# Performance work log

Hardware: AMD Instinct MI355X
Metric: run time of the kernel (lower is better)

Reference implementation:

```python
import jax, jax.numpy as jnp
import numpy as np

N_NODES = 100000  # same count for users and items
N_EDGES = 4000000
D = 64
EPS = 1e-12


def setup_inputs() -> dict:
    key = jax.random.key(0)
    ks = jax.random.split(key, 8)
    return {
        "user_feat": jax.random.normal(ks[0], (N_NODES, D), dtype=jnp.float32),
        "item_feat": jax.random.normal(ks[1], (N_NODES, D), dtype=jnp.float32),
        "norm_ui": jax.random.uniform(ks[2], (N_EDGES, 1), dtype=jnp.float32),
        "norm_iu": jax.random.uniform(ks[3], (N_EDGES, 1), dtype=jnp.float32),
        "src_ui": jax.random.randint(ks[4], (N_EDGES,), 0, N_NODES, dtype=jnp.int32),
        "dst_ui": jax.random.randint(ks[5], (N_EDGES,), 0, N_NODES, dtype=jnp.int32),
        "src_iu": jax.random.randint(ks[6], (N_EDGES,), 0, N_NODES, dtype=jnp.int32),
        "dst_iu": jax.random.randint(ks[7], (N_EDGES,), 0, N_NODES, dtype=jnp.int32),
    }


def _l2_normalize(x):
    # F.normalize(x, dim=1, p=2): x / max(||x||_2, eps)
    n = jnp.sqrt(jnp.sum(x * x, axis=1, keepdims=True))
    return x / jnp.maximum(n, EPS)


def reference(user_feat, item_feat, norm_ui, norm_iu, src_ui, dst_ui, src_iu, dst_iu):
    # per-edge gather + scale (messages), then scatter-sum to destination nodes
    item_h = jax.ops.segment_sum(norm_ui * user_feat[src_ui], dst_ui, num_segments=N_NODES)
    user_h = jax.ops.segment_sum(norm_iu * item_feat[src_iu], dst_iu, num_segments=N_NODES)
    # per-node-type L2 normalize; stack [user_h, item_h] -> [2, N, D]
    return jnp.stack([_l2_normalize(user_h), _l2_normalize(item_h)])
```

## Files before the change

kernel.cpp:

```cpp
#include <hip/hip_runtime.h>

#define DFEAT 64
#define EPS 1e-12f
#define BPB 64
#define MAXB 3200
#define QPT 4
#define LSORT_CAP 3264


__device__ __forceinline__ unsigned pack_src_w(int s, float w) {
    unsigned u = __float_as_uint(w) + 0x8000u;
    return (((u >> 16) & 0x7FFFu) << 17) | (unsigned)s;
}
__device__ __forceinline__ int unpack_src(unsigned p) { return (int)(p & 0x1FFFFu); }
__device__ __forceinline__ float unpack_w(unsigned p) {
    return __uint_as_float(((p >> 17) & 0x7FFFu) << 16);
}

__global__ void zero_int_kernel(int* __restrict__ p, int n) {
    int i = blockIdx.x * blockDim.x + threadIdx.x;
    if (i < n) p[i] = 0;
}

__global__ __launch_bounds__(256, 6) void partition_kernel(
        const int* __restrict__ src_ui,
        const int* __restrict__ dst_ui,
        const float* __restrict__ norm_ui,
        const int* __restrict__ src_iu,
        const int* __restrict__ dst_iu,
        const float* __restrict__ norm_iu,
        int* __restrict__ cursor,
        unsigned* __restrict__ srcw,
        unsigned char* __restrict__ binlo,
        int n_edges, int n_nodes,
        int nbuckets, int cap) {
    __shared__ int cnt[MAXB];
    __shared__ int basearr[MAXB];
    const int tid = threadIdx.x;
    const long long total = 2LL * n_edges;
    const long long qbase = (long long)blockIdx.x * (256 * QPT);

    for (int c = tid; c < nbuckets; c += 256) cnt[c] = 0;
    __syncthreads();

    for (int k = 0; k < QPT; ++k) {
        long long q = qbase + (long long)k * 256 + tid;
        long long g0 = q << 2;
        if (g0 >= total) continue;
        if (g0 + 3 < total && (g0 + 3 < n_edges || g0 >= n_edges)) {
            const bool iu = (g0 >= n_edges);
            long long e0 = iu ? (g0 - n_edges) : g0;
            int4 d = *reinterpret_cast<const int4*>((iu ? dst_iu : dst_ui) + e0);
            int boff = iu ? n_nodes : 0;
            atomicAdd(&cnt[(d.x + boff) >> 6], 1);
            atomicAdd(&cnt[(d.y + boff) >> 6], 1);
            atomicAdd(&cnt[(d.z + boff) >> 6], 1);
            atomicAdd(&cnt[(d.w + boff) >> 6], 1);
        } else {
            for (long long g = g0; g < g0 + 4 && g < total; ++g) {
                int bin = (g < n_edges) ? dst_ui[g]
                                        : n_nodes + dst_iu[g - n_edges];
                atomicAdd(&cnt[bin >> 6], 1);
            }
        }
    }
    __syncthreads();

    for (int c = tid; c < nbuckets; c += 256) {
        int n = cnt[c];
        basearr[c] = (n > 0) ? atomicAdd(&cursor[c], n) : 0;
    }
    __syncthreads();
    for (int c = tid; c < nbuckets; c += 256) cnt[c] = 0;
    __syncthreads();

    auto place = [&](int bin, int s, float w) {
        int bu = bin >> 6;
        int r = atomicAdd(&cnt[bu], 1);
        int pos = basearr[bu] + r;
        if (pos < cap) {
            long long slot = (long long)bu * cap + pos;
            srcw[slot] = pack_src_w(s, w);
            binlo[slot] = (unsigned char)(bin & 63);
        }
    };
    for (int k = 0; k < QPT; ++k) {
        long long q = qbase + (long long)k * 256 + tid;
        long long g0 = q << 2;
        if (g0 >= total) continue;
        if (g0 + 3 < total && (g0 + 3 < n_edges || g0 >= n_edges)) {
            const bool iu = (g0 >= n_edges);
            long long e0 = iu ? (g0 - n_edges) : g0;
            int4 d = *reinterpret_cast<const int4*>((iu ? dst_iu : dst_ui) + e0);
            int4 s = *reinterpret_cast<const int4*>((iu ? src_iu : src_ui) + e0);
            float4 w = *reinterpret_cast<const float4*>((iu ? norm_iu : norm_ui) + e0);
            int boff = iu ? n_nodes : 0;
            place(d.x + boff, s.x, w.x);
            place(d.y + boff, s.y, w.y);
            place(d.z + boff, s.z, w.z);
            place(d.w + boff, s.w, w.w);
        } else {
            for (long long g = g0; g < g0 + 4 && g < total; ++g) {
                int bin, s; float w;
                if (g < n_edges) {
                    bin = dst_ui[g]; s = src_ui[g]; w = norm_ui[g];
                } else {
                    long long e = g - n_edges;
                    bin = n_nodes + dst_iu[e]; s = src_iu[e]; w = norm_iu[e];
                }
                place(bin, s, w);
            }
        }
    }
}

__global__ __launch_bounds__(256, 8) void bucket_sort_gather_kernel(
    const float* __restrict__ user_feat,
    const float* __restrict__ item_feat,
    const int* __restrict__ cursor,
    const unsigned* __restrict__ srcw,
    const unsigned char* __restrict__ binlo,
    float* __restrict__ out, int n_nodes, int cap) {
    __shared__ unsigned lsort[LSORT_CAP];
    __shared__ int cnt[BPB];
    __shared__ int cnt2[BPB];
    __shared__ int rowptr[BPB + 1];
    const int tid = threadIdx.x;
    const int lane = tid & 63;
    const int wid = tid >> 6;
    const int c = blockIdx.x;

    int m = cursor[c];
    if (m > cap) m = cap;
    const long long base = (long long)c * cap;

    if (tid < BPB) { cnt[tid] = 0; cnt2[tid] = 0; }
    __syncthreads();

    for (int i = tid * 4; i < m; i += 1024) {
        if (i + 3 < m) {
            uchar4 b = *reinterpret_cast<const uchar4*>(binlo + base + i);
            atomicAdd(&cnt[(int)b.x], 1);
            atomicAdd(&cnt[(int)b.y], 1);
            atomicAdd(&cnt[(int)b.z], 1);
            atomicAdd(&cnt[(int)b.w], 1);
        } else {
            for (int k = i; k < m; ++k) atomicAdd(&cnt[(int)binlo[base + k]], 1);
        }
    }
    __syncthreads();

    if (wid == 0) {
        int v = cnt[lane];
        int s = v;
        #pragma unroll
        for (int off = 1; off < 64; off <<= 1) {
            int y = __shfl_up(s, off, 64);
            if (lane >= off) s += y;
        }
        rowptr[lane] = s - v;
        if (lane == 63) rowptr[BPB] = s;
    }
    __syncthreads();

    for (int i = tid * 4; i < m; i += 1024) {
        if (i + 3 < m) {
            uint4 sv = *reinterpret_cast<const uint4*>(srcw + base + i);
            uchar4 b = *reinterpret_cast<const uchar4*>(binlo + base + i);
            int p0 = rowptr[(int)b.x] + atomicAdd(&cnt2[(int)b.x], 1);
            lsort[p0] = sv.x;
            int p1 = rowptr[(int)b.y] + atomicAdd(&cnt2[(int)b.y], 1);
            lsort[p1] = sv.y;
            int p2 = rowptr[(int)b.z] + atomicAdd(&cnt2[(int)b.z], 1);
            lsort[p2] = sv.z;
            int p3 = rowptr[(int)b.w] + atomicAdd(&cnt2[(int)b.w], 1);
            lsort[p3] = sv.w;
        } else {
            for (int k = i; k < m; ++k) {
                int b = (int)binlo[base + k];
                int pos = rowptr[b] + atomicAdd(&cnt2[b], 1);
                lsort[pos] = srcw[base + k];
            }
        }
    }
    __syncthreads();

    const int n_bins = 2 * n_nodes;
    for (int r = wid; r < BPB; r += 4) {
        int bin_global = c * BPB + r;
        if (bin_global >= n_bins) break;
        const float* feat = (bin_global < n_nodes) ? user_feat : item_feat;
        int js = rowptr[r];
        int je = rowptr[r + 1];
        float acc = 0.f;
        int j = js;
        for (; j + 8 <= je; j += 8) {
            unsigned s0 = lsort[j + 0];
            unsigned s1 = lsort[j + 1];
            unsigned s2 = lsort[j + 2];
            unsigned s3 = lsort[j + 3];
            unsigned s4 = lsort[j + 4];
            unsigned s5 = lsort[j + 5];
            unsigned s6 = lsort[j + 6];
            unsigned s7 = lsort[j + 7];
            float f0 = feat[(long long)unpack_src(s0) * DFEAT + lane];
            float f1 = feat[(long long)unpack_src(s1) * DFEAT + lane];
            float f2 = feat[(long long)unpack_src(s2) * DFEAT + lane];
            float f3 = feat[(long long)unpack_src(s3) * DFEAT + lane];
            float f4 = feat[(long long)unpack_src(s4) * DFEAT + lane];
            float f5 = feat[(long long)unpack_src(s5) * DFEAT + lane];
            float f6 = feat[(long long)unpack_src(s6) * DFEAT + lane];
            float f7 = feat[(long long)unpack_src(s7) * DFEAT + lane];
            acc += unpack_w(s0) * f0;
            acc += unpack_w(s1) * f1;
            acc += unpack_w(s2) * f2;
            acc += unpack_w(s3) * f3;
            acc += unpack_w(s4) * f4;
            acc += unpack_w(s5) * f5;
            acc += unpack_w(s6) * f6;
            acc += unpack_w(s7) * f7;
        }
        for (; j < je; ++j) {
            unsigned s = lsort[j];
            acc += unpack_w(s) * feat[(long long)unpack_src(s) * DFEAT + lane];
        }
        float ss = acc * acc;
        #pragma unroll
        for (int o = 32; o > 0; o >>= 1) ss += __shfl_xor(ss, o, 64);
        float scale = 1.0f / fmaxf(sqrtf(ss), EPS);
        int out_row = (bin_global < n_nodes) ? (bin_global + n_nodes)
                                             : (bin_global - n_nodes);
        out[(long long)out_row * DFEAT + lane] = acc * scale;
    }
}


__global__ void zero_f32_kernel(float* __restrict__ p, int n4) {
    int i = blockIdx.x * blockDim.x + threadIdx.x;
    if (i < n4) reinterpret_cast<float4*>(p)[i] = make_float4(0.f, 0.f, 0.f, 0.f);
}

__global__ void scatter_edges_kernel(const float* __restrict__ user_feat,
                                     const float* __restrict__ item_feat,
                                     const float* __restrict__ norm_ui,
                                     const float* __restrict__ norm_iu,
                                     const int* __restrict__ src_ui,
                                     const int* __restrict__ dst_ui,
                                     const int* __restrict__ src_iu,
                                     const int* __restrict__ dst_iu,
                                     float* __restrict__ user_acc,
                                     float* __restrict__ item_acc,
                                     int n_edges) {
    long long idx = (long long)blockIdx.x * blockDim.x + threadIdx.x;
    int e = (int)(idx >> 6);
    int d = (int)(idx & 63);
    if (e < n_edges) {
        int s = src_ui[e];
        int t = dst_ui[e];
        atomicAdd(&item_acc[(long long)t * DFEAT + d],
                  norm_ui[e] * user_feat[(long long)s * DFEAT + d]);
    } else {
        e -= n_edges;
        if (e < n_edges) {
            int s = src_iu[e];
            int t = dst_iu[e];
            atomicAdd(&user_acc[(long long)t * DFEAT + d],
                      norm_iu[e] * item_feat[(long long)s * DFEAT + d]);
        }
    }
}

__global__ void normalize_rows_kernel(float* __restrict__ buf, int n_rows) {
    int gid = blockIdx.x * blockDim.x + threadIdx.x;
    int row = gid >> 6;
    int lane = gid & 63;
    if (row >= n_rows) return;
    long long off = (long long)row * DFEAT + lane;
    float x = buf[off];
    float ss = x * x;
    #pragma unroll
    for (int o = 32; o > 0; o >>= 1) ss += __shfl_xor(ss, o, 64);
    float scale = 1.0f / fmaxf(sqrtf(ss), EPS);
    buf[off] = x * scale;
}

extern "C" void kernel_launch(void* const* d_in, const int* in_sizes, int n_in,
                              void* d_out, int out_size, void* d_ws, size_t ws_size,
                              hipStream_t stream) {
    const float* user_feat = (const float*)d_in[0];
    const float* item_feat = (const float*)d_in[1];
    const float* norm_ui   = (const float*)d_in[2];
    const float* norm_iu   = (const float*)d_in[3];
    const int* src_ui = (const int*)d_in[4];
    const int* dst_ui = (const int*)d_in[5];
    const int* src_iu = (const int*)d_in[6];
    const int* dst_iu = (const int*)d_in[7];

    const int n_nodes = in_sizes[0] / DFEAT;
    const int n_edges = in_sizes[4];
    const int n_bins  = 2 * n_nodes;
    const int nbuckets = (n_bins + BPB - 1) / BPB;

    const size_t head_bytes = (((size_t)nbuckets * 4) + 255) & ~(size_t)255;
    long long cap_ll = 0;
    if (ws_size > head_bytes) {
        cap_ll = (long long)((ws_size - head_bytes) / ((size_t)nbuckets * 5));
        cap_ll &= ~15LL;
    }
    if (cap_ll > LSORT_CAP) cap_ll = LSORT_CAP;
    const long long mean_per_bucket = 2LL * n_edges / (nbuckets > 0 ? nbuckets : 1);
    const long long cap_needed = mean_per_bucket + mean_per_bucket / 4 + 64;
    const int cap = (int)cap_ll;

    if (nbuckets <= MAXB && n_nodes <= (1 << 17) && cap_ll >= cap_needed) {
        int* cursor = (int*)d_ws;
        unsigned* srcw = (unsigned*)((char*)d_ws + head_bytes);
        unsigned char* binlo = (unsigned char*)((char*)srcw + (size_t)nbuckets * cap * 4);

        zero_int_kernel<<<(nbuckets + 255) / 256, 256, 0, stream>>>(cursor, nbuckets);
        long long total = 2LL * n_edges;
        long long rpb = 256LL * QPT * 4;
        int pblocks = (int)((total + rpb - 1) / rpb);
        partition_kernel<<<pblocks, 256, 0, stream>>>(
            src_ui, dst_ui, norm_ui, src_iu, dst_iu, norm_iu,
            cursor, srcw, binlo, n_edges, n_nodes, nbuckets, cap);
        bucket_sort_gather_kernel<<<nbuckets, 256, 0, stream>>>(
            user_feat, item_feat, cursor, srcw, binlo,
            (float*)d_out, n_nodes, cap);
    } else {
        float* user_acc = (float*)d_out;
        float* item_acc = user_acc + (size_t)n_nodes * DFEAT;
        const int n4 = out_size / 4;
        zero_f32_kernel<<<(n4 + 255) / 256, 256, 0, stream>>>(user_acc, n4);
        const long long total_threads = 2LL * n_edges * DFEAT;
        scatter_edges_kernel<<<(int)((total_threads + 255) / 256), 256, 0, stream>>>(
            user_feat, item_feat, norm_ui, norm_iu,
            src_ui, dst_ui, src_iu, dst_iu, user_acc, item_acc, n_edges);
        const long long norm_threads = (long long)n_bins * DFEAT;
        normalize_rows_kernel<<<(int)((norm_threads + 255) / 256), 256, 0, stream>>>(
            user_acc, n_bins);
    }
}
```

Before: 638.1 us.

## Replace fixed-capacity buckets with exact two-level counting sort into CSR

The single partition pass into fixed-capacity per-bucket slots, followed by an LDS sort fused with the gather, is replaced by an exact two-level radix partition. A coarse histogram and scan (256 nodes per bucket) set exact offsets, stage A scatters packed edges into coarse buckets, stage B sorts each bucket by fine bin into a global CSR, and a separate kernel does the per-row gather and normalize. This drops the capacity padding and the overflow risk, and it borrows the output buffer as scratch. In exchange it adds kernel launches and an extra global round trip over the edges. The new path is guarded by an `out_size`-in-bytes check that may not hold if `out_size` counts elements, which would send execution to the slow atomic fallback.

```diff
diff --git a/kernel.cpp b/kernel.cpp
--- a/kernel.cpp
+++ b/kernel.cpp
@@ -2,10 +2,9 @@
 
 #define DFEAT 64
 #define EPS 1e-12f
-#define BPB 64
-#define MAXB 3200
+#define BPB_C 256
+#define MAXC 800
 #define QPT 4
-#define LSORT_CAP 3264
 
 
 __device__ __forceinline__ unsigned pack_src_w(int s, float w) {
@@ -22,25 +21,17 @@
     if (i < n) p[i] = 0;
 }
 
-__global__ __launch_bounds__(256, 6) void partition_kernel(
-        const int* __restrict__ src_ui,
+__global__ __launch_bounds__(256, 6) void coarse_hist_kernel(
         const int* __restrict__ dst_ui,
-        const float* __restrict__ norm_ui,
-        const int* __restrict__ src_iu,
         const int* __restrict__ dst_iu,
-        const float* __restrict__ norm_iu,
-        int* __restrict__ cursor,
-        unsigned* __restrict__ srcw,
-        unsigned char* __restrict__ binlo,
-        int n_edges, int n_nodes,
-        int nbuckets, int cap) {
-    __shared__ int cnt[MAXB];
-    __shared__ int basearr[MAXB];
+        int* __restrict__ cntC,
+        int n_edges, int n_nodes, int nbC) {
+    __shared__ int cnt[MAXC];
     const int tid = threadIdx.x;
     const long long total = 2LL * n_edges;
     const long long qbase = (long long)blockIdx.x * (256 * QPT);
 
-    for (int c = tid; c < nbuckets; c += 256) cnt[c] = 0;
+    for (int c = tid; c < nbC; c += 256) cnt[c] = 0;
     __syncthreads();
 
     for (int k = 0; k < QPT; ++k) {
@@ -52,37 +43,104 @@
             long long e0 = iu ? (g0 - n_edges) : g0;
             int4 d = *reinterpret_cast<const int4*>((iu ? dst_iu : dst_ui) + e0);
             int boff = iu ? n_nodes : 0;
-            atomicAdd(&cnt[(d.x + boff) >> 6], 1);
-            atomicAdd(&cnt[(d.y + boff) >> 6], 1);
-            atomicAdd(&cnt[(d.z + boff) >> 6], 1);
-            atomicAdd(&cnt[(d.w + boff) >> 6], 1);
+            atomicAdd(&cnt[(d.x + boff) >> 8], 1);
+            atomicAdd(&cnt[(d.y + boff) >> 8], 1);
+            atomicAdd(&cnt[(d.z + boff) >> 8], 1);
+            atomicAdd(&cnt[(d.w + boff) >> 8], 1);
         } else {
             for (long long g = g0; g < g0 + 4 && g < total; ++g) {
                 int bin = (g < n_edges) ? dst_ui[g]
                                         : n_nodes + dst_iu[g - n_edges];
-                atomicAdd(&cnt[bin >> 6], 1);
+                atomicAdd(&cnt[bin >> 8], 1);
             }
         }
     }
     __syncthreads();
-
-    for (int c = tid; c < nbuckets; c += 256) {
+    for (int c = tid; c < nbC; c += 256) {
         int n = cnt[c];
-        basearr[c] = (n > 0) ? atomicAdd(&cursor[c], n) : 0;
-    }
-    __syncthreads();
-    for (int c = tid; c < nbuckets; c += 256) cnt[c] = 0;
+        if (n > 0) atomicAdd(&cntC[c], n);
+    }
+}
+
+__global__ void coarse_scan_kernel(const int* __restrict__ cntC,
+                                   int* __restrict__ rowptrC,
+                                   int* __restrict__ cursorC,
+                                   int* __restrict__ rowptrF,
+                                   int nbC, int n_bins) {
+    __shared__ int s[1024];
+    const int tid = threadIdx.x;
+    int v = (tid < nbC) ? cntC[tid] : 0;
+    s[tid] = v;
+    __syncthreads();
+    for (int off = 1; off < 1024; off <<= 1) {
+        int y = (tid >= off) ? s[tid - off] : 0;
+        __syncthreads();
+        s[tid] += y;
+        __syncthreads();
+    }
+    int incl = s[tid];
+    int excl = incl - v;
+    if (tid < nbC) { rowptrC[tid] = excl; cursorC[tid] = excl; }
+    if (tid == nbC - 1) { rowptrC[nbC] = incl; rowptrF[n_bins] = incl; }
+}
+
+__global__ __launch_bounds__(256, 6) void stageA_kernel(
+        const int* __restrict__ src_ui,
+        const int* __restrict__ dst_ui,
+        const float* __restrict__ norm_ui,
+        const int* __restrict__ src_iu,
+        const int* __restrict__ dst_iu,
+        const float* __restrict__ norm_iu,
+        int* __restrict__ cursorC,
+        unsigned* __restrict__ srcwA,
+        unsigned char* __restrict__ binA,
+        int n_edges, int n_nodes, int nbC) {
+    __shared__ int cnt[MAXC];
+    __shared__ int basearr[MAXC];
+    const int tid = threadIdx.x;
+    const long long total = 2LL * n_edges;
+    const long long qbase = (long long)blockIdx.x * (256 * QPT);
+
+    for (int c = tid; c < nbC; c += 256) cnt[c] = 0;
+    __syncthreads();
+
+    for (int k = 0; k < QPT; ++k) {
+        long long q = qbase + (long long)k * 256 + tid;
+        long long g0 = q << 2;
+        if (g0 >= total) continue;
+        if (g0 + 3 < total && (g0 + 3 < n_edges || g0 >= n_edges)) {
+            const bool iu = (g0 >= n_edges);
+            long long e0 = iu ? (g0 - n_edges) : g0;
+            int4 d = *reinterpret_cast<const int4*>((iu ? dst_iu : dst_ui) + e0);
+            int boff = iu ? n_nodes : 0;
+            atomicAdd(&cnt[(d.x + boff) >> 8], 1);
+            atomicAdd(&cnt[(d.y + boff) >> 8], 1);
+            atomicAdd(&cnt[(d.z + boff) >> 8], 1);
+            atomicAdd(&cnt[(d.w + boff) >> 8], 1);
+        } else {
+            for (long long g = g0; g < g0 + 4 && g < total; ++g) {
+                int bin = (g < n_edges) ? dst_ui[g]
+                                        : n_nodes + dst_iu[g - n_edges];
+                atomicAdd(&cnt[bin >> 8], 1);
+            }
+        }
+    }
+    __syncthreads();
+
+    for (int c = tid; c < nbC; c += 256) {
+        int n = cnt[c];
+        basearr[c] = (n > 0) ? atomicAdd(&cursorC[c], n) : 0;
+    }
+    __syncthreads();
+    for (int c = tid; c < nbC; c += 256) cnt[c] = 0;
     __syncthreads();
 
     auto place = [&](int bin, int s, float w) {
-        int bu = bin >> 6;
+        int bu = bin >> 8;
         int r = atomicAdd(&cnt[bu], 1);
         int pos = basearr[bu] + r;
-        if (pos < cap) {
-            long long slot = (long long)bu * cap + pos;
-            srcw[slot] = pack_src_w(s, w);
-            binlo[slot] = (unsigned char)(bin & 63);
-        }
+        srcwA[pos] = pack_src_w(s, w);
+        binA[pos] = (unsigned char)(bin & 255);
     };
     for (int k = 0; k < QPT; ++k) {
         long long q = qbase + (long long)k * 256 + tid;
@@ -114,124 +172,110 @@
     }
 }
 
-__global__ __launch_bounds__(256, 8) void bucket_sort_gather_kernel(
-    const float* __restrict__ user_feat,
-    const float* __restrict__ item_feat,
-    const int* __restrict__ cursor,
-    const unsigned* __restrict__ srcw,
-    const unsigned char* __restrict__ binlo,
-    float* __restrict__ out, int n_nodes, int cap) {
-    __shared__ unsigned lsort[LSORT_CAP];
-    __shared__ int cnt[BPB];
-    __shared__ int cnt2[BPB];
-    __shared__ int rowptr[BPB + 1];
+__global__ __launch_bounds__(256, 8) void stageB_kernel(
+        const int* __restrict__ rowptrC,
+        const unsigned* __restrict__ srcwA,
+        const unsigned char* __restrict__ binA,
+        unsigned* __restrict__ srcwB,
+        int* __restrict__ rowptrF,
+        int n_bins) {
+    __shared__ int cnt[BPB_C];
+    __shared__ int cnt2[BPB_C];
+    __shared__ int rp[BPB_C];
+    __shared__ int wtot[4];
     const int tid = threadIdx.x;
     const int lane = tid & 63;
     const int wid = tid >> 6;
     const int c = blockIdx.x;
-
-    int m = cursor[c];
-    if (m > cap) m = cap;
-    const long long base = (long long)c * cap;
-
-    if (tid < BPB) { cnt[tid] = 0; cnt2[tid] = 0; }
-    __syncthreads();
-
-    for (int i = tid * 4; i < m; i += 1024) {
-        if (i + 3 < m) {
-            uchar4 b = *reinterpret_cast<const uchar4*>(binlo + base + i);
-            atomicAdd(&cnt[(int)b.x], 1);
-            atomicAdd(&cnt[(int)b.y], 1);
-            atomicAdd(&cnt[(int)b.z], 1);
-            atomicAdd(&cnt[(int)b.w], 1);
-        } else {
-            for (int k = i; k < m; ++k) atomicAdd(&cnt[(int)binlo[base + k]], 1);
-        }
-    }
-    __syncthreads();
-
-    if (wid == 0) {
-        int v = cnt[lane];
+    const int js = rowptrC[c];
+    const int je = rowptrC[c + 1];
+
+    cnt[tid] = 0; cnt2[tid] = 0;
+    __syncthreads();
+
+    for (int i = js + tid; i < je; i += 256)
+        atomicAdd(&cnt[(int)binA[i]], 1);
+    __syncthreads();
+
+    {
+        int v = cnt[tid];
         int s = v;
         #pragma unroll
         for (int off = 1; off < 64; off <<= 1) {
             int y = __shfl_up(s, off, 64);
             if (lane >= off) s += y;
         }
-        rowptr[lane] = s - v;
-        if (lane == 63) rowptr[BPB] = s;
-    }
-    __syncthreads();
-
-    for (int i = tid * 4; i < m; i += 1024) {
-        if (i + 3 < m) {
-            uint4 sv = *reinterpret_cast<const uint4*>(srcw + base + i);
-            uchar4 b = *reinterpret_cast<const uchar4*>(binlo + base + i);
-            int p0 = rowptr[(int)b.x] + atomicAdd(&cnt2[(int)b.x], 1);
-            lsort[p0] = sv.x;
-            int p1 = rowptr[(int)b.y] + atomicAdd(&cnt2[(int)b.y], 1);
-            lsort[p1] = sv.y;
-            int p2 = rowptr[(int)b.z] + atomicAdd(&cnt2[(int)b.z], 1);
-            lsort[p2] = sv.z;
-            int p3 = rowptr[(int)b.w] + atomicAdd(&cnt2[(int)b.w], 1);
-            lsort[p3] = sv.w;
-        } else {
-            for (int k = i; k < m; ++k) {
-                int b = (int)binlo[base + k];
-                int pos = rowptr[b] + atomicAdd(&cnt2[b], 1);
-                lsort[pos] = srcw[base + k];
-            }
-        }
-    }
-    __syncthreads();
-
+        if (lane == 63) wtot[wid] = s;
+        __syncthreads();
+        int add = 0;
+        for (int w = 0; w < wid; ++w) add += wtot[w];
+        rp[tid] = add + s - v;
+    }
+    __syncthreads();
+
+    int bg = c * BPB_C + tid;
+    if (bg < n_bins) rowptrF[bg] = js + rp[tid];
+
+    for (int i = js + tid; i < je; i += 256) {
+        int b = (int)binA[i];
+        int pos = js + rp[b] + atomicAdd(&cnt2[b], 1);
+        srcwB[pos] = srcwA[i];
+    }
+}
+
+__global__ __launch_bounds__(256, 8) void csr_gather_kernel(
+    const float* __restrict__ user_feat,
+    const float* __restrict__ item_feat,
+    const int* __restrict__ rowptr,
+    const unsigned* __restrict__ srcw,
+    float* __restrict__ out, int n_nodes) {
+    const int tid = threadIdx.x;
+    const int lane = tid & 63;
+    const int wid = tid >> 6;
     const int n_bins = 2 * n_nodes;
-    for (int r = wid; r < BPB; r += 4) {
-        int bin_global = c * BPB + r;
-        if (bin_global >= n_bins) break;
-        const float* feat = (bin_global < n_nodes) ? user_feat : item_feat;
-        int js = rowptr[r];
-        int je = rowptr[r + 1];
-        float acc = 0.f;
-        int j = js;
-        for (; j + 8 <= je; j += 8) {
-            unsigned s0 = lsort[j + 0];
-            unsigned s1 = lsort[j + 1];
-            unsigned s2 = lsort[j + 2];
-            unsigned s3 = lsort[j + 3];
-            unsigned s4 = lsort[j + 4];
-            unsigned s5 = lsort[j + 5];
-            unsigned s6 = lsort[j + 6];
-            unsigned s7 = lsort[j + 7];
-            float f0 = feat[(long long)unpack_src(s0) * DFEAT + lane];
-            float f1 = feat[(long long)unpack_src(s1) * DFEAT + lane];
-            float f2 = feat[(long long)unpack_src(s2) * DFEAT + lane];
-            float f3 = feat[(long long)unpack_src(s3) * DFEAT + lane];
-            float f4 = feat[(long long)unpack_src(s4) * DFEAT + lane];
-            float f5 = feat[(long long)unpack_src(s5) * DFEAT + lane];
-            float f6 = feat[(long long)unpack_src(s6) * DFEAT + lane];
-            float f7 = feat[(long long)unpack_src(s7) * DFEAT + lane];
-            acc += unpack_w(s0) * f0;
-            acc += unpack_w(s1) * f1;
-            acc += unpack_w(s2) * f2;
-            acc += unpack_w(s3) * f3;
-            acc += unpack_w(s4) * f4;
-            acc += unpack_w(s5) * f5;
-            acc += unpack_w(s6) * f6;
-            acc += unpack_w(s7) * f7;
-        }
-        for (; j < je; ++j) {
-            unsigned s = lsort[j];
-            acc += unpack_w(s) * feat[(long long)unpack_src(s) * DFEAT + lane];
-        }
-        float ss = acc * acc;
-        #pragma unroll
-        for (int o = 32; o > 0; o >>= 1) ss += __shfl_xor(ss, o, 64);
-        float scale = 1.0f / fmaxf(sqrtf(ss), EPS);
-        int out_row = (bin_global < n_nodes) ? (bin_global + n_nodes)
-                                             : (bin_global - n_nodes);
-        out[(long long)out_row * DFEAT + lane] = acc * scale;
-    }
+    const int r = blockIdx.x * 4 + wid;
+    if (r >= n_bins) return;
+    const float* feat = (r < n_nodes) ? user_feat : item_feat;
+    const int js = rowptr[r];
+    const int je = rowptr[r + 1];
+    float acc = 0.f;
+    int j = js;
+    for (; j + 8 <= je; j += 8) {
+        unsigned s0 = srcw[j + 0];
+        unsigned s1 = srcw[j + 1];
+        unsigned s2 = srcw[j + 2];
+        unsigned s3 = srcw[j + 3];
+        unsigned s4 = srcw[j + 4];
+        unsigned s5 = srcw[j + 5];
+        unsigned s6 = srcw[j + 6];
+        unsigned s7 = srcw[j + 7];
+        float f0 = feat[(long long)unpack_src(s0) * DFEAT + lane];
+        float f1 = feat[(long long)unpack_src(s1) * DFEAT + lane];
+        float f2 = feat[(long long)unpack_src(s2) * DFEAT + lane];
+        float f3 = feat[(long long)unpack_src(s3) * DFEAT + lane];
+        float f4 = feat[(long long)unpack_src(s4) * DFEAT + lane];
+        float f5 = feat[(long long)unpack_src(s5) * DFEAT + lane];
+        float f6 = feat[(long long)unpack_src(s6) * DFEAT + lane];
+        float f7 = feat[(long long)unpack_src(s7) * DFEAT + lane];
+        acc += unpack_w(s0) * f0;
+        acc += unpack_w(s1) * f1;
+        acc += unpack_w(s2) * f2;
+        acc += unpack_w(s3) * f3;
+        acc += unpack_w(s4) * f4;
+        acc += unpack_w(s5) * f5;
+        acc += unpack_w(s6) * f6;
+        acc += unpack_w(s7) * f7;
+    }
+    for (; j < je; ++j) {
+        unsigned s = srcw[j];
+        acc += unpack_w(s) * feat[(long long)unpack_src(s) * DFEAT + lane];
+    }
+    float ss = acc * acc;
+    #pragma unroll
+    for (int o = 32; o > 0; o >>= 1) ss += __shfl_xor(ss, o, 64);
+    float scale = 1.0f / fmaxf(sqrtf(ss), EPS);
+    int out_row = (r < n_nodes) ? (r + n_nodes) : (r - n_nodes);
+    out[(long long)out_row * DFEAT + lane] = acc * scale;
 }
 
 
@@ -299,34 +343,43 @@
     const int n_nodes = in_sizes[0] / DFEAT;
     const int n_edges = in_sizes[4];
     const int n_bins  = 2 * n_nodes;
-    const int nbuckets = (n_bins + BPB - 1) / BPB;
-
-    const size_t head_bytes = (((size_t)nbuckets * 4) + 255) & ~(size_t)255;
-    long long cap_ll = 0;
-    if (ws_size > head_bytes) {
-        cap_ll = (long long)((ws_size - head_bytes) / ((size_t)nbuckets * 5));
-        cap_ll &= ~15LL;
-    }
-    if (cap_ll > LSORT_CAP) cap_ll = LSORT_CAP;
-    const long long mean_per_bucket = 2LL * n_edges / (nbuckets > 0 ? nbuckets : 1);
-    const long long cap_needed = mean_per_bucket + mean_per_bucket / 4 + 64;
-    const int cap = (int)cap_ll;
-
-    if (nbuckets <= MAXB && n_nodes <= (1 << 17) && cap_ll >= cap_needed) {
-        int* cursor = (int*)d_ws;
-        unsigned* srcw = (unsigned*)((char*)d_ws + head_bytes);
-        unsigned char* binlo = (unsigned char*)((char*)srcw + (size_t)nbuckets * cap * 4);
-
-        zero_int_kernel<<<(nbuckets + 255) / 256, 256, 0, stream>>>(cursor, nbuckets);
-        long long total = 2LL * n_edges;
-        long long rpb = 256LL * QPT * 4;
-        int pblocks = (int)((total + rpb - 1) / rpb);
-        partition_kernel<<<pblocks, 256, 0, stream>>>(
+    const int nbC     = (n_bins + BPB_C - 1) / BPB_C;
+    const long long total = 2LL * n_edges;
+
+    auto align256 = [](size_t x) { return (x + 255) & ~(size_t)255; };
+    const size_t o_cntC  = 0;
+    const size_t o_rpC   = align256(o_cntC + (size_t)nbC * 4);
+    const size_t o_curC  = align256(o_rpC + ((size_t)nbC + 1) * 4);
+    const size_t o_rpF   = align256(o_curC + (size_t)nbC * 4);
+    const size_t o_srcwB = align256(o_rpF + ((size_t)n_bins + 1) * 4);
+    const size_t ws_need = o_srcwB + (size_t)total * 4;
+    const size_t out_need = (size_t)total * 5;
+
+    if (nbC <= MAXC && nbC <= 1024 && n_nodes <= (1 << 17) &&
+        ws_size >= ws_need && (size_t)out_size >= out_need) {
+        int* cntC       = (int*)((char*)d_ws + o_cntC);
+        int* rowptrC    = (int*)((char*)d_ws + o_rpC);
+        int* cursorC    = (int*)((char*)d_ws + o_curC);
+        int* rowptrF    = (int*)((char*)d_ws + o_rpF);
+        unsigned* srcwB = (unsigned*)((char*)d_ws + o_srcwB);
+        unsigned* srcwA      = (unsigned*)d_out;
+        unsigned char* binA  = (unsigned char*)d_out + (size_t)total * 4;
+
+        const long long rpb = 256LL * QPT * 4;
+        const int pblocks = (int)((total + rpb - 1) / rpb);
+
+        zero_int_kernel<<<(nbC + 255) / 256, 256, 0, stream>>>(cntC, nbC);
+        coarse_hist_kernel<<<pblocks, 256, 0, stream>>>(
+            dst_ui, dst_iu, cntC, n_edges, n_nodes, nbC);
+        coarse_scan_kernel<<<1, 1024, 0, stream>>>(
+            cntC, rowptrC, cursorC, rowptrF, nbC, n_bins);
+        stageA_kernel<<<pblocks, 256, 0, stream>>>(
             src_ui, dst_ui, norm_ui, src_iu, dst_iu, norm_iu,
-            cursor, srcw, binlo, n_edges, n_nodes, nbuckets, cap);
-        bucket_sort_gather_kernel<<<nbuckets, 256, 0, stream>>>(
-            user_feat, item_feat, cursor, srcw, binlo,
-            (float*)d_out, n_nodes, cap);
+            cursorC, srcwA, binA, n_edges, n_nodes, nbC);
+        stageB_kernel<<<nbC, 256, 0, stream>>>(
+            rowptrC, srcwA, binA, srcwB, rowptrF, n_bins);
+        csr_gather_kernel<<<(n_bins + 3) / 4, 256, 0, stream>>>(
+            user_feat, item_feat, rowptrF, srcwB, (float*)d_out, n_nodes);
     } else {
         float* user_acc = (float*)d_out;
         float* item_acc = user_acc + (size_t)n_nodes * DFEAT;
```

Result: slower. 2.097 ms (+228.6%).
